# Kernel optimization log

Measured on AMD Instinct MI355X. Metric: run time of the kernel, lower is better.

## Reference

```python
import jax, jax.numpy as jnp
import numpy as np

N_NODES = 50000
N_EDGES = 600000
D_IN = 128
D_HID = 128


def _sage_conv(x, src, dst, W_l, b_l, W_r):
    """PyG SAGEConv (mean aggr): out = lin_l(mean_{j in N(i)} x_j) + lin_r(x_i).
    bias lives in lin_l only."""
    n = x.shape[0]
    agg = jax.ops.segment_sum(x[src], dst, num_segments=n)            # [N, D]
    cnt = jax.ops.segment_sum(jnp.ones((src.shape[0],), x.dtype), dst, num_segments=n)
    mean = agg / jnp.maximum(cnt, 1.0)[:, None]
    return mean @ W_l.T + b_l + x @ W_r.T


def setup_inputs() -> dict:
    key = jax.random.key(0)
    ks = jax.random.split(key, 8)
    glorot = lambda k, o, i: jax.random.normal(k, (o, i), jnp.float32) * np.sqrt(2.0 / (o + i))
    return {
        "x": jax.random.normal(ks[0], (N_NODES, D_IN), jnp.float32),
        "edge_index": jax.random.randint(ks[1], (2, N_EDGES), 0, N_NODES, jnp.int64),
        "W1_l": glorot(ks[2], D_HID, D_IN),
        "b1": jnp.zeros((D_HID,), jnp.float32),
        "W1_r": glorot(ks[3], D_HID, D_IN),
        "W2_l": glorot(ks[4], D_HID, D_HID),
        "b2": jnp.zeros((D_HID,), jnp.float32),
        "W2_r": glorot(ks[5], D_HID, D_HID),
    }


def reference(x, edge_index, W1_l, b1, W1_r, W2_l, b2, W2_r):
    src, dst = edge_index[0], edge_index[1]
    h = _sage_conv(x, src, dst, W1_l, b1, W1_r)
    h = jax.nn.leaky_relu(h, negative_slope=0.2)
    return _sage_conv(h, src, dst, W2_l, b2, W2_r)
```

## Files before the change

### kernel.cpp

```cpp
#include <hip/hip_runtime.h>

#define N_NODES 50000
#define N_EDGES 600000
#define D 128
#define CAP 64

typedef __attribute__((ext_vector_type(8))) short bf16x8;
typedef __attribute__((ext_vector_type(4))) float floatx4;

__device__ inline unsigned int f2bf(float f) {
    unsigned int u = __float_as_uint(f);
    return (u + 0x7FFFu + ((u >> 16) & 1u)) >> 16;
}
__device__ inline float bf_lo(unsigned int u) { return __uint_as_float(u << 16); }
__device__ inline float bf_hi(unsigned int u) { return __uint_as_float(u & 0xFFFF0000u); }

__global__ void k_prep(const float* __restrict__ x, unsigned short* __restrict__ xbf,
                       const float* __restrict__ wa, const float* __restrict__ wb,
                       const float* __restrict__ wc, const float* __restrict__ wd,
                       unsigned short* __restrict__ wbf,
                       const int* __restrict__ src, const int* __restrict__ dst,
                       int* __restrict__ cnt, unsigned short* __restrict__ buf,
                       int* __restrict__ spillN, int* __restrict__ spillD,
                       int* __restrict__ spillS) {
    const int b = blockIdx.x;
    const int t = threadIdx.x;
    if (b < 2344) {
        int e = b * 256 + t;
        if (e < N_EDGES) {
            int d = dst[e], s = src[e];
            int p = atomicAdd(&cnt[d], 1);
            if (p < CAP) {
                buf[(size_t)d * CAP + p] = (unsigned short)s;
            } else {
                int k = atomicAdd(spillN, 1);
                spillD[k] = d; spillS[k] = s;
            }
        }
    } else if (b < 8594) {
        int i = (b - 2344) * 256 + t;
        float4 v = ((const float4*)x)[i];
        uint2 o;
        o.x = f2bf(v.x) | (f2bf(v.y) << 16);
        o.y = f2bf(v.z) | (f2bf(v.w) << 16);
        ((uint2*)xbf)[i] = o;
    } else {
        int i = (b - 8594) * 256 + t;
        const float* srcs[4] = {wa, wb, wc, wd};
        wbf[i] = (unsigned short)f2bf(srcs[i >> 14][i & 16383]);
    }
}

#define ACC8(vv) do { \
    acc[0] += bf_lo((vv).x); acc[1] += bf_hi((vv).x); \
    acc[2] += bf_lo((vv).y); acc[3] += bf_hi((vv).y); \
    acc[4] += bf_lo((vv).z); acc[5] += bf_hi((vv).z); \
    acc[6] += bf_lo((vv).w); acc[7] += bf_hi((vv).w); } while (0)

template <bool RELU, bool OUT_BF16>
__global__ void __launch_bounds__(256) k_gather_layer(
    const int* __restrict__ cnt, const unsigned short* __restrict__ buf,
    const int* __restrict__ spillN, const int* __restrict__ spillD,
    const int* __restrict__ spillS,
    const unsigned short* __restrict__ Xbf,
    const unsigned short* __restrict__ Wlbf, const float* __restrict__ bias,
    const unsigned short* __restrict__ Wrbf, void* __restrict__ outp) {
    __shared__ unsigned short tile[16][136];

    const int t = threadIdx.x;
    const int node0 = blockIdx.x * 16;

    {
        const int nl = t >> 4, q = t & 15;
        const int node = node0 + nl;
        const int deg = cnt[node];
        const int m = deg < CAP ? deg : CAP;
        const unsigned short* __restrict__ nb = buf + (size_t)node * CAP;
        float acc[8] = {0.f, 0.f, 0.f, 0.f, 0.f, 0.f, 0.f, 0.f};
        int e = 0;
        for (; e + 8 <= m; e += 8) {
            uint4 v[8];
#pragma unroll
            for (int u = 0; u < 8; ++u)
                v[u] = *(const uint4*)(Xbf + (size_t)nb[e + u] * D + q * 8);
#pragma unroll
            for (int u = 0; u < 8; ++u) ACC8(v[u]);
        }
        for (; e + 4 <= m; e += 4) {
            uint4 v[4];
#pragma unroll
            for (int u = 0; u < 4; ++u)
                v[u] = *(const uint4*)(Xbf + (size_t)nb[e + u] * D + q * 8);
#pragma unroll
            for (int u = 0; u < 4; ++u) ACC8(v[u]);
        }
        for (; e < m; ++e) {
            uint4 v = *(const uint4*)(Xbf + (size_t)nb[e] * D + q * 8);
            ACC8(v);
        }
        if (deg > CAP) {
            int sn = *spillN;
            for (int k = 0; k < sn; ++k) {
                if (spillD[k] == node) {
                    uint4 v = *(const uint4*)(Xbf + (size_t)spillS[k] * D + q * 8);
                    ACC8(v);
                }
            }
        }
        float inv = (deg > 0) ? 1.0f / (float)deg : 0.0f;
        uint4 o;
        o.x = f2bf(acc[0] * inv) | (f2bf(acc[1] * inv) << 16);
        o.y = f2bf(acc[2] * inv) | (f2bf(acc[3] * inv) << 16);
        o.z = f2bf(acc[4] * inv) | (f2bf(acc[5] * inv) << 16);
        o.w = f2bf(acc[6] * inv) | (f2bf(acc[7] * inv) << 16);
        *(uint4*)(&tile[nl][q * 8]) = o;
    }
    __syncthreads();

    const int lane = t & 63;
    const int wv = t >> 6;
    const int l15 = lane & 15;
    const int quad = lane >> 4;

    floatx4 c0 = (floatx4)(0.f), c1 = (floatx4)(0.f);
    const int nf0 = wv * 2, nf1 = wv * 2 + 1;

    const unsigned short* mrow = &tile[l15][quad * 8];
    const unsigned short* arowX = Xbf + (size_t)(node0 + l15) * D + quad * 8;

#pragma unroll
    for (int kk = 0; kk < 4; ++kk) {
        bf16x8 a = *(const bf16x8*)(mrow + kk * 32);
        bf16x8 b0 = *(const bf16x8*)(Wlbf + (size_t)(nf0 * 16 + l15) * D + kk * 32 + quad * 8);
        bf16x8 b1 = *(const bf16x8*)(Wlbf + (size_t)(nf1 * 16 + l15) * D + kk * 32 + quad * 8);
        c0 = __builtin_amdgcn_mfma_f32_16x16x32_bf16(a, b0, c0, 0, 0, 0);
        c1 = __builtin_amdgcn_mfma_f32_16x16x32_bf16(a, b1, c1, 0, 0, 0);
    }
#pragma unroll
    for (int kk = 0; kk < 4; ++kk) {
        bf16x8 a = *(const bf16x8*)(arowX + kk * 32);
        bf16x8 b0 = *(const bf16x8*)(Wrbf + (size_t)(nf0 * 16 + l15) * D + kk * 32 + quad * 8);
        bf16x8 b1 = *(const bf16x8*)(Wrbf + (size_t)(nf1 * 16 + l15) * D + kk * 32 + quad * 8);
        c0 = __builtin_amdgcn_mfma_f32_16x16x32_bf16(a, b0, c0, 0, 0, 0);
        c1 = __builtin_amdgcn_mfma_f32_16x16x32_bf16(a, b1, c1, 0, 0, 0);
    }

#pragma unroll
    for (int j = 0; j < 2; ++j) {
        floatx4 c = j ? c1 : c0;
        int f = (wv * 2 + j) * 16 + l15;
        float bv = bias[f];
#pragma unroll
        for (int r = 0; r < 4; ++r) {
            float v = c[r] + bv;
            if (RELU) v = v > 0.f ? v : 0.2f * v;
            int node = node0 + quad * 4 + r;
            if (OUT_BF16)
                ((unsigned short*)outp)[(size_t)node * D + f] = (unsigned short)f2bf(v);
            else
                ((float*)outp)[(size_t)node * D + f] = v;
        }
    }
}


extern "C" void kernel_launch(void* const* d_in, const int* in_sizes, int n_in,
                              void* d_out, int out_size, void* d_ws, size_t ws_size,
                              hipStream_t stream) {
    (void)in_sizes; (void)n_in; (void)out_size; (void)ws_size;

    const float* x   = (const float*)d_in[0];
    const int*   ei  = (const int*)d_in[1];
    const float* W1l = (const float*)d_in[2];
    const float* b1  = (const float*)d_in[3];
    const float* W1r = (const float*)d_in[4];
    const float* W2l = (const float*)d_in[5];
    const float* b2  = (const float*)d_in[6];
    const float* W2r = (const float*)d_in[7];

    const int* src = ei;
    const int* dst = ei + N_EDGES;

    char* ws = (char*)d_ws;
    int* cnt              = (int*)(ws + 0);
    int* spillN           = (int*)(ws + 200000);
    int* spillD           = (int*)(ws + 200064);
    int* spillS           = (int*)(ws + 2600064);
    unsigned short* buf   = (unsigned short*)(ws + 5000064);
    unsigned short* wbf   = (unsigned short*)(ws + 11400064);
    unsigned short* hbf   = (unsigned short*)(ws + 11531136);

    unsigned short* xbf = (unsigned short*)d_out;
    float* out = (float*)d_out;

    unsigned short* w1l_bf = wbf;
    unsigned short* w1r_bf = wbf + 16384;
    unsigned short* w2l_bf = wbf + 32768;
    unsigned short* w2r_bf = wbf + 49152;

    hipMemsetAsync(ws, 0, 200064, stream);

    k_prep<<<8850, 256, 0, stream>>>(x, xbf, W1l, W1r, W2l, W2r, wbf,
                                     src, dst, cnt, buf, spillN, spillD, spillS);

    k_gather_layer<true, true><<<N_NODES / 16, 256, 0, stream>>>(
        cnt, buf, spillN, spillD, spillS, xbf, w1l_bf, b1, w1r_bf, (void*)hbf);
    k_gather_layer<false, false><<<N_NODES / 16, 256, 0, stream>>>(
        cnt, buf, spillN, spillD, spillS, hbf, w2l_bf, b2, w2r_bf, (void*)out);
}
```

Baseline: 223.7 us.

## Gather each node's neighbours with a full wavefront split four ways

The gather phase now gives each destination node a whole 64-lane wavefront, with 1024 threads per block, instead of 16 lanes. Each group of 16 lanes sums a quarter of the node's neighbour list, and the partial sums are combined with cross-lane shuffles. Neighbour ids are first staged in shared memory. The aim is more independent gather loads in flight per node, to hide random-access latency. In exchange, only a quarter of the threads take part in the MFMA projection, and the aggressive launch bounds may cap registers and cause spills.

Result: slower. 241.7 us (+8.1%).

```diff
diff --git a/kernel.cpp b/kernel.cpp
--- a/kernel.cpp
+++ b/kernel.cpp
@@ -58,7 +58,7 @@
     acc[6] += bf_lo((vv).w); acc[7] += bf_hi((vv).w); } while (0)
 
 template <bool RELU, bool OUT_BF16>
-__global__ void __launch_bounds__(256) k_gather_layer(
+__global__ void __launch_bounds__(1024, 8) k_gather_layer(
     const int* __restrict__ cnt, const unsigned short* __restrict__ buf,
     const int* __restrict__ spillN, const int* __restrict__ spillD,
     const int* __restrict__ spillS,
@@ -66,39 +66,46 @@
     const unsigned short* __restrict__ Wlbf, const float* __restrict__ bias,
     const unsigned short* __restrict__ Wrbf, void* __restrict__ outp) {
     __shared__ unsigned short tile[16][136];
+    __shared__ unsigned short lds_ids[16][64];
 
     const int t = threadIdx.x;
     const int node0 = blockIdx.x * 16;
 
     {
-        const int nl = t >> 4, q = t & 15;
-        const int node = node0 + nl;
+        const int wid = t >> 6;
+        const int lane = t & 63;
+        const int q = lane & 15;
+        const int par = lane >> 4;
+        const int node = node0 + wid;
         const int deg = cnt[node];
         const int m = deg < CAP ? deg : CAP;
-        const unsigned short* __restrict__ nb = buf + (size_t)node * CAP;
+
+        lds_ids[wid][lane] = buf[(size_t)node * CAP + lane];
+        const unsigned short* idr = &lds_ids[wid][0];
+
+        const int lo = (m * par) >> 2;
+        const int hi = (m * (par + 1)) >> 2;
+
         float acc[8] = {0.f, 0.f, 0.f, 0.f, 0.f, 0.f, 0.f, 0.f};
-        int e = 0;
-        for (; e + 8 <= m; e += 8) {
-            uint4 v[8];
-#pragma unroll
-            for (int u = 0; u < 8; ++u)
-                v[u] = *(const uint4*)(Xbf + (size_t)nb[e + u] * D + q * 8);
-#pragma unroll
-            for (int u = 0; u < 8; ++u) ACC8(v[u]);
-        }
-        for (; e + 4 <= m; e += 4) {
-            uint4 v[4];
-#pragma unroll
-            for (int u = 0; u < 4; ++u)
-                v[u] = *(const uint4*)(Xbf + (size_t)nb[e + u] * D + q * 8);
-#pragma unroll
-            for (int u = 0; u < 4; ++u) ACC8(v[u]);
-        }
-        for (; e < m; ++e) {
-            uint4 v = *(const uint4*)(Xbf + (size_t)nb[e] * D + q * 8);
-            ACC8(v);
-        }
-        if (deg > CAP) {
+        int e = lo;
+        for (; e + 4 <= hi; e += 4) {
+            uint4 v0 = *(const uint4*)(Xbf + (size_t)idr[e] * D + q * 8);
+            uint4 v1 = *(const uint4*)(Xbf + (size_t)idr[e + 1] * D + q * 8);
+            uint4 v2 = *(const uint4*)(Xbf + (size_t)idr[e + 2] * D + q * 8);
+            uint4 v3 = *(const uint4*)(Xbf + (size_t)idr[e + 3] * D + q * 8);
+            ACC8(v0); ACC8(v1); ACC8(v2); ACC8(v3);
+        }
+        {
+            int r = hi - e;
+            uint4 v0, v1, v2;
+            if (r > 0) v0 = *(const uint4*)(Xbf + (size_t)idr[e] * D + q * 8);
+            if (r > 1) v1 = *(const uint4*)(Xbf + (size_t)idr[e + 1] * D + q * 8);
+            if (r > 2) v2 = *(const uint4*)(Xbf + (size_t)idr[e + 2] * D + q * 8);
+            if (r > 0) ACC8(v0);
+            if (r > 1) ACC8(v1);
+            if (r > 2) ACC8(v2);
+        }
+        if (deg > CAP && par == 0) {
             int sn = *spillN;
             for (int k = 0; k < sn; ++k) {
                 if (spillD[k] == node) {
@@ -107,58 +114,67 @@
                 }
             }
         }
-        float inv = (deg > 0) ? 1.0f / (float)deg : 0.0f;
-        uint4 o;
-        o.x = f2bf(acc[0] * inv) | (f2bf(acc[1] * inv) << 16);
-        o.y = f2bf(acc[2] * inv) | (f2bf(acc[3] * inv) << 16);
-        o.z = f2bf(acc[4] * inv) | (f2bf(acc[5] * inv) << 16);
-        o.w = f2bf(acc[6] * inv) | (f2bf(acc[7] * inv) << 16);
-        *(uint4*)(&tile[nl][q * 8]) = o;
+#pragma unroll
+        for (int i = 0; i < 8; ++i) {
+            acc[i] += __shfl_xor(acc[i], 16, 64);
+            acc[i] += __shfl_xor(acc[i], 32, 64);
+        }
+        if (lane < 16) {
+            float inv = (deg > 0) ? 1.0f / (float)deg : 0.0f;
+            uint4 o;
+            o.x = f2bf(acc[0] * inv) | (f2bf(acc[1] * inv) << 16);
+            o.y = f2bf(acc[2] * inv) | (f2bf(acc[3] * inv) << 16);
+            o.z = f2bf(acc[4] * inv) | (f2bf(acc[5] * inv) << 16);
+            o.w = f2bf(acc[6] * inv) | (f2bf(acc[7] * inv) << 16);
+            *(uint4*)(&tile[wid][q * 8]) = o;
+        }
     }
     __syncthreads();
 
-    const int lane = t & 63;
-    const int wv = t >> 6;
-    const int l15 = lane & 15;
-    const int quad = lane >> 4;
-
-    floatx4 c0 = (floatx4)(0.f), c1 = (floatx4)(0.f);
-    const int nf0 = wv * 2, nf1 = wv * 2 + 1;
-
-    const unsigned short* mrow = &tile[l15][quad * 8];
-    const unsigned short* arowX = Xbf + (size_t)(node0 + l15) * D + quad * 8;
-
-#pragma unroll
-    for (int kk = 0; kk < 4; ++kk) {
-        bf16x8 a = *(const bf16x8*)(mrow + kk * 32);
-        bf16x8 b0 = *(const bf16x8*)(Wlbf + (size_t)(nf0 * 16 + l15) * D + kk * 32 + quad * 8);
-        bf16x8 b1 = *(const bf16x8*)(Wlbf + (size_t)(nf1 * 16 + l15) * D + kk * 32 + quad * 8);
-        c0 = __builtin_amdgcn_mfma_f32_16x16x32_bf16(a, b0, c0, 0, 0, 0);
-        c1 = __builtin_amdgcn_mfma_f32_16x16x32_bf16(a, b1, c1, 0, 0, 0);
-    }
-#pragma unroll
-    for (int kk = 0; kk < 4; ++kk) {
-        bf16x8 a = *(const bf16x8*)(arowX + kk * 32);
-        bf16x8 b0 = *(const bf16x8*)(Wrbf + (size_t)(nf0 * 16 + l15) * D + kk * 32 + quad * 8);
-        bf16x8 b1 = *(const bf16x8*)(Wrbf + (size_t)(nf1 * 16 + l15) * D + kk * 32 + quad * 8);
-        c0 = __builtin_amdgcn_mfma_f32_16x16x32_bf16(a, b0, c0, 0, 0, 0);
-        c1 = __builtin_amdgcn_mfma_f32_16x16x32_bf16(a, b1, c1, 0, 0, 0);
-    }
-
-#pragma unroll
-    for (int j = 0; j < 2; ++j) {
-        floatx4 c = j ? c1 : c0;
-        int f = (wv * 2 + j) * 16 + l15;
-        float bv = bias[f];
-#pragma unroll
-        for (int r = 0; r < 4; ++r) {
-            float v = c[r] + bv;
-            if (RELU) v = v > 0.f ? v : 0.2f * v;
-            int node = node0 + quad * 4 + r;
-            if (OUT_BF16)
-                ((unsigned short*)outp)[(size_t)node * D + f] = (unsigned short)f2bf(v);
-            else
-                ((float*)outp)[(size_t)node * D + f] = v;
+    if (t < 256) {
+        const int lane = t & 63;
+        const int wv = t >> 6;
+        const int l15 = lane & 15;
+        const int quad = lane >> 4;
+
+        floatx4 c0 = (floatx4)(0.f), c1 = (floatx4)(0.f);
+        const int nf0 = wv * 2, nf1 = wv * 2 + 1;
+
+        const unsigned short* mrow = &tile[l15][quad * 8];
+        const unsigned short* arowX = Xbf + (size_t)(node0 + l15) * D + quad * 8;
+
+#pragma unroll
+        for (int kk = 0; kk < 4; ++kk) {
+            bf16x8 a = *(const bf16x8*)(mrow + kk * 32);
+            bf16x8 b0 = *(const bf16x8*)(Wlbf + (size_t)(nf0 * 16 + l15) * D + kk * 32 + quad * 8);
+            bf16x8 b1 = *(const bf16x8*)(Wlbf + (size_t)(nf1 * 16 + l15) * D + kk * 32 + quad * 8);
+            c0 = __builtin_amdgcn_mfma_f32_16x16x32_bf16(a, b0, c0, 0, 0, 0);
+            c1 = __builtin_amdgcn_mfma_f32_16x16x32_bf16(a, b1, c1, 0, 0, 0);
+        }
+#pragma unroll
+        for (int kk = 0; kk < 4; ++kk) {
+            bf16x8 a = *(const bf16x8*)(arowX + kk * 32);
+            bf16x8 b0 = *(const bf16x8*)(Wrbf + (size_t)(nf0 * 16 + l15) * D + kk * 32 + quad * 8);
+            bf16x8 b1 = *(const bf16x8*)(Wrbf + (size_t)(nf1 * 16 + l15) * D + kk * 32 + quad * 8);
+            c0 = __builtin_amdgcn_mfma_f32_16x16x32_bf16(a, b0, c0, 0, 0, 0);
+            c1 = __builtin_amdgcn_mfma_f32_16x16x32_bf16(a, b1, c1, 0, 0, 0);
+        }
+
+#pragma unroll
+        for (int j = 0; j < 2; ++j) {
+            floatx4 c = j ? c1 : c0;
+            int f = (wv * 2 + j) * 16 + l15;
+            float bv = bias[f];
+#pragma unroll
+            for (int r = 0; r < 4; ++r) {
+                float v = c[r] + bv;
+                if (RELU) v = v > 0.f ? v : 0.2f * v;
+                int node = node0 + quad * 4 + r;
+                if (OUT_BF16)
+                    ((unsigned short*)outp)[(size_t)node * D + f] = (unsigned short)f2bf(v);
+                else
+                    ((float*)outp)[(size_t)node * D + f] = v;
+            }
         }
     }
 }
@@ -203,8 +219,8 @@
     k_prep<<<8850, 256, 0, stream>>>(x, xbf, W1l, W1r, W2l, W2r, wbf,
                                      src, dst, cnt, buf, spillN, spillD, spillS);
 
-    k_gather_layer<true, true><<<N_NODES / 16, 256, 0, stream>>>(
+    k_gather_layer<true, true><<<N_NODES / 16, 1024, 0, stream>>>(
         cnt, buf, spillN, spillD, spillS, xbf, w1l_bf, b1, w1r_bf, (void*)hbf);
-    k_gather_layer<false, false><<<N_NODES / 16, 256, 0, stream>>>(
+    k_gather_layer<false, false><<<N_NODES / 16, 1024, 0, stream>>>(
         cnt, buf, spillN, spillD, spillS, hbf, w2l_bf, b2, w2r_bf, (void*)out);
 }
```

## Fuse prep and both SAGE layers into one persistent cooperative kernel

Applied to the files above, without the earlier changes.

Replaces the memset plus three kernel launches with a single cooperative persistent kernel that zeroes the counters, builds the adjacency buckets, converts inputs to bf16, and runs both layers. The phases are separated by grid-wide syncs, and tiles are processed in grid-stride loops. This removes launch gaps and the separate memset, at the cost of grid barrier overhead and a grid capped by occupancy (at most 2048 blocks). A fallback to the old multi-kernel path remains if the cooperative launch fails.

Result: slower. 509.9 us (+128.0%).

```diff
diff --git a/kernel.cpp b/kernel.cpp
--- a/kernel.cpp
+++ b/kernel.cpp
@@ -1,9 +1,14 @@
 #include <hip/hip_runtime.h>
+#include <hip/hip_cooperative_groups.h>
+
+namespace cg = cooperative_groups;
 
 #define N_NODES 50000
 #define N_EDGES 600000
 #define D 128
 #define CAP 64
+#define NTILES (N_NODES / 16)
+#define SCAN_BLOCKS ((N_NODES + 255) / 256)
 
 typedef __attribute__((ext_vector_type(8))) short bf16x8;
 typedef __attribute__((ext_vector_type(4))) float floatx4;
@@ -14,6 +19,179 @@
 }
 __device__ inline float bf_lo(unsigned int u) { return __uint_as_float(u << 16); }
 __device__ inline float bf_hi(unsigned int u) { return __uint_as_float(u & 0xFFFF0000u); }
+
+#define ACC8(vv) do { \
+    acc[0] += bf_lo((vv).x); acc[1] += bf_hi((vv).x); \
+    acc[2] += bf_lo((vv).y); acc[3] += bf_hi((vv).y); \
+    acc[4] += bf_lo((vv).z); acc[5] += bf_hi((vv).z); \
+    acc[6] += bf_lo((vv).w); acc[7] += bf_hi((vv).w); } while (0)
+
+template <bool RELU, bool OUT_BF16>
+__device__ void layer_tile(int tileId, unsigned short (*tile)[136],
+                           const int* __restrict__ cnt, const unsigned short* __restrict__ buf,
+                           const int* __restrict__ spillN, const int* __restrict__ spillD,
+                           const int* __restrict__ spillS,
+                           const unsigned short* __restrict__ Xbf,
+                           const unsigned short* __restrict__ Wlbf, const float* __restrict__ bias,
+                           const unsigned short* __restrict__ Wrbf, void* __restrict__ outp) {
+    const int t = threadIdx.x;
+    const int node0 = tileId * 16;
+
+    {
+        const int nl = t >> 4, q = t & 15;
+        const int node = node0 + nl;
+        const int deg = cnt[node];
+        const int m = deg < CAP ? deg : CAP;
+        const unsigned short* __restrict__ nb = buf + (size_t)node * CAP;
+        float acc[8] = {0.f, 0.f, 0.f, 0.f, 0.f, 0.f, 0.f, 0.f};
+        int e = 0;
+        for (; e + 8 <= m; e += 8) {
+            uint4 v[8];
+#pragma unroll
+            for (int u = 0; u < 8; ++u)
+                v[u] = *(const uint4*)(Xbf + (size_t)nb[e + u] * D + q * 8);
+#pragma unroll
+            for (int u = 0; u < 8; ++u) ACC8(v[u]);
+        }
+        for (; e + 4 <= m; e += 4) {
+            uint4 v[4];
+#pragma unroll
+            for (int u = 0; u < 4; ++u)
+                v[u] = *(const uint4*)(Xbf + (size_t)nb[e + u] * D + q * 8);
+#pragma unroll
+            for (int u = 0; u < 4; ++u) ACC8(v[u]);
+        }
+        for (; e < m; ++e) {
+            uint4 v = *(const uint4*)(Xbf + (size_t)nb[e] * D + q * 8);
+            ACC8(v);
+        }
+        if (deg > CAP) {
+            int sn = *spillN;
+            for (int k = 0; k < sn; ++k) {
+                if (spillD[k] == node) {
+                    uint4 v = *(const uint4*)(Xbf + (size_t)spillS[k] * D + q * 8);
+                    ACC8(v);
+                }
+            }
+        }
+        float inv = (deg > 0) ? 1.0f / (float)deg : 0.0f;
+        uint4 o;
+        o.x = f2bf(acc[0] * inv) | (f2bf(acc[1] * inv) << 16);
+        o.y = f2bf(acc[2] * inv) | (f2bf(acc[3] * inv) << 16);
+        o.z = f2bf(acc[4] * inv) | (f2bf(acc[5] * inv) << 16);
+        o.w = f2bf(acc[6] * inv) | (f2bf(acc[7] * inv) << 16);
+        *(uint4*)(&tile[nl][q * 8]) = o;
+    }
+    __syncthreads();
+
+    {
+        const int lane = t & 63;
+        const int wv = t >> 6;
+        const int l15 = lane & 15;
+        const int quad = lane >> 4;
+
+        floatx4 c0 = (floatx4)(0.f), c1 = (floatx4)(0.f);
+        const int nf0 = wv * 2, nf1 = wv * 2 + 1;
+
+        const unsigned short* mrow = &tile[l15][quad * 8];
+        const unsigned short* arowX = Xbf + (size_t)(node0 + l15) * D + quad * 8;
+
+#pragma unroll
+        for (int kk = 0; kk < 4; ++kk) {
+            bf16x8 a = *(const bf16x8*)(mrow + kk * 32);
+            bf16x8 b0 = *(const bf16x8*)(Wlbf + (size_t)(nf0 * 16 + l15) * D + kk * 32 + quad * 8);
+            bf16x8 b1 = *(const bf16x8*)(Wlbf + (size_t)(nf1 * 16 + l15) * D + kk * 32 + quad * 8);
+            c0 = __builtin_amdgcn_mfma_f32_16x16x32_bf16(a, b0, c0, 0, 0, 0);
+            c1 = __builtin_amdgcn_mfma_f32_16x16x32_bf16(a, b1, c1, 0, 0, 0);
+        }
+#pragma unroll
+        for (int kk = 0; kk < 4; ++kk) {
+            bf16x8 a = *(const bf16x8*)(arowX + kk * 32);
+            bf16x8 b0 = *(const bf16x8*)(Wrbf + (size_t)(nf0 * 16 + l15) * D + kk * 32 + quad * 8);
+            bf16x8 b1 = *(const bf16x8*)(Wrbf + (size_t)(nf1 * 16 + l15) * D + kk * 32 + quad * 8);
+            c0 = __builtin_amdgcn_mfma_f32_16x16x32_bf16(a, b0, c0, 0, 0, 0);
+            c1 = __builtin_amdgcn_mfma_f32_16x16x32_bf16(a, b1, c1, 0, 0, 0);
+        }
+
+#pragma unroll
+        for (int j = 0; j < 2; ++j) {
+            floatx4 c = j ? c1 : c0;
+            int f = (wv * 2 + j) * 16 + l15;
+            float bv = bias[f];
+#pragma unroll
+            for (int r = 0; r < 4; ++r) {
+                float v = c[r] + bv;
+                if (RELU) v = v > 0.f ? v : 0.2f * v;
+                int node = node0 + quad * 4 + r;
+                if (OUT_BF16)
+                    ((unsigned short*)outp)[(size_t)node * D + f] = (unsigned short)f2bf(v);
+                else
+                    ((float*)outp)[(size_t)node * D + f] = v;
+            }
+        }
+    }
+    __syncthreads();
+}
+
+__global__ void __launch_bounds__(256, 8) k_fused(
+    const float* __restrict__ x, const int* __restrict__ src, const int* __restrict__ dst,
+    const float* __restrict__ W1l, const float* __restrict__ b1, const float* __restrict__ W1r,
+    const float* __restrict__ W2l, const float* __restrict__ b2, const float* __restrict__ W2r,
+    int* __restrict__ cnt, unsigned short* __restrict__ buf,
+    int* __restrict__ spillN, int* __restrict__ spillD, int* __restrict__ spillS,
+    unsigned short* __restrict__ wbf, unsigned short* xbf,
+    unsigned short* __restrict__ hbf, float* out) {
+    __shared__ unsigned short tile[16][136];
+
+    cg::grid_group grid = cg::this_grid();
+    const int t = threadIdx.x;
+    const int gid = blockIdx.x * 256 + t;
+    const int gsz = gridDim.x * 256;
+
+    for (int i = gid; i < N_NODES; i += gsz) cnt[i] = 0;
+    if (gid == 0) *spillN = 0;
+    __threadfence();
+    grid.sync();
+    __threadfence();
+
+    for (int e = gid; e < N_EDGES; e += gsz) {
+        int d = dst[e], s = src[e];
+        int p = atomicAdd(&cnt[d], 1);
+        if (p < CAP) {
+            buf[(size_t)d * CAP + p] = (unsigned short)s;
+        } else {
+            int k = atomicAdd(spillN, 1);
+            spillD[k] = d; spillS[k] = s;
+        }
+    }
+    for (int i = gid; i < N_NODES * D / 4; i += gsz) {
+        float4 v = ((const float4*)x)[i];
+        uint2 o;
+        o.x = f2bf(v.x) | (f2bf(v.y) << 16);
+        o.y = f2bf(v.z) | (f2bf(v.w) << 16);
+        ((uint2*)xbf)[i] = o;
+    }
+    for (int i = gid; i < 4 * D * D; i += gsz) {
+        int wsel = i >> 14, idx = i & 16383;
+        const float* p = wsel == 0 ? W1l : wsel == 1 ? W1r : wsel == 2 ? W2l : W2r;
+        wbf[i] = (unsigned short)f2bf(p[idx]);
+    }
+    __threadfence();
+    grid.sync();
+    __threadfence();
+
+    for (int tl = blockIdx.x; tl < NTILES; tl += gridDim.x)
+        layer_tile<true, true>(tl, tile, cnt, buf, spillN, spillD, spillS,
+                               xbf, wbf, b1, wbf + 16384, (void*)hbf);
+    __threadfence();
+    grid.sync();
+    __threadfence();
+
+    for (int tl = blockIdx.x; tl < NTILES; tl += gridDim.x)
+        layer_tile<false, false>(tl, tile, cnt, buf, spillN, spillD, spillS,
+                                 hbf, wbf + 32768, b2, wbf + 49152, (void*)out);
+}
+
 
 __global__ void k_prep(const float* __restrict__ x, unsigned short* __restrict__ xbf,
                        const float* __restrict__ wa, const float* __restrict__ wb,
@@ -51,12 +229,6 @@
     }
 }
 
-#define ACC8(vv) do { \
-    acc[0] += bf_lo((vv).x); acc[1] += bf_hi((vv).x); \
-    acc[2] += bf_lo((vv).y); acc[3] += bf_hi((vv).y); \
-    acc[4] += bf_lo((vv).z); acc[5] += bf_hi((vv).z); \
-    acc[6] += bf_lo((vv).w); acc[7] += bf_hi((vv).w); } while (0)
-
 template <bool RELU, bool OUT_BF16>
 __global__ void __launch_bounds__(256) k_gather_layer(
     const int* __restrict__ cnt, const unsigned short* __restrict__ buf,
@@ -66,101 +238,8 @@
     const unsigned short* __restrict__ Wlbf, const float* __restrict__ bias,
     const unsigned short* __restrict__ Wrbf, void* __restrict__ outp) {
     __shared__ unsigned short tile[16][136];
-
-    const int t = threadIdx.x;
-    const int node0 = blockIdx.x * 16;
-
-    {
-        const int nl = t >> 4, q = t & 15;
-        const int node = node0 + nl;
-        const int deg = cnt[node];
-        const int m = deg < CAP ? deg : CAP;
-        const unsigned short* __restrict__ nb = buf + (size_t)node * CAP;
-        float acc[8] = {0.f, 0.f, 0.f, 0.f, 0.f, 0.f, 0.f, 0.f};
-        int e = 0;
-        for (; e + 8 <= m; e += 8) {
-            uint4 v[8];
-#pragma unroll
-            for (int u = 0; u < 8; ++u)
-                v[u] = *(const uint4*)(Xbf + (size_t)nb[e + u] * D + q * 8);
-#pragma unroll
-            for (int u = 0; u < 8; ++u) ACC8(v[u]);
-        }
-        for (; e + 4 <= m; e += 4) {
-            uint4 v[4];
-#pragma unroll
-            for (int u = 0; u < 4; ++u)
-                v[u] = *(const uint4*)(Xbf + (size_t)nb[e + u] * D + q * 8);
-#pragma unroll
-            for (int u = 0; u < 4; ++u) ACC8(v[u]);
-        }
-        for (; e < m; ++e) {
-            uint4 v = *(const uint4*)(Xbf + (size_t)nb[e] * D + q * 8);
-            ACC8(v);
-        }
-        if (deg > CAP) {
-            int sn = *spillN;
-            for (int k = 0; k < sn; ++k) {
-                if (spillD[k] == node) {
-                    uint4 v = *(const uint4*)(Xbf + (size_t)spillS[k] * D + q * 8);
-                    ACC8(v);
-                }
-            }
-        }
-        float inv = (deg > 0) ? 1.0f / (float)deg : 0.0f;
-        uint4 o;
-        o.x = f2bf(acc[0] * inv) | (f2bf(acc[1] * inv) << 16);
-        o.y = f2bf(acc[2] * inv) | (f2bf(acc[3] * inv) << 16);
-        o.z = f2bf(acc[4] * inv) | (f2bf(acc[5] * inv) << 16);
-        o.w = f2bf(acc[6] * inv) | (f2bf(acc[7] * inv) << 16);
-        *(uint4*)(&tile[nl][q * 8]) = o;
-    }
-    __syncthreads();
-
-    const int lane = t & 63;
-    const int wv = t >> 6;
-    const int l15 = lane & 15;
-    const int quad = lane >> 4;
-
-    floatx4 c0 = (floatx4)(0.f), c1 = (floatx4)(0.f);
-    const int nf0 = wv * 2, nf1 = wv * 2 + 1;
-
-    const unsigned short* mrow = &tile[l15][quad * 8];
-    const unsigned short* arowX = Xbf + (size_t)(node0 + l15) * D + quad * 8;
-
-#pragma unroll
-    for (int kk = 0; kk < 4; ++kk) {
-        bf16x8 a = *(const bf16x8*)(mrow + kk * 32);
-        bf16x8 b0 = *(const bf16x8*)(Wlbf + (size_t)(nf0 * 16 + l15) * D + kk * 32 + quad * 8);
-        bf16x8 b1 = *(const bf16x8*)(Wlbf + (size_t)(nf1 * 16 + l15) * D + kk * 32 + quad * 8);
-        c0 = __builtin_amdgcn_mfma_f32_16x16x32_bf16(a, b0, c0, 0, 0, 0);
-        c1 = __builtin_amdgcn_mfma_f32_16x16x32_bf16(a, b1, c1, 0, 0, 0);
-    }
-#pragma unroll
-    for (int kk = 0; kk < 4; ++kk) {
-        bf16x8 a = *(const bf16x8*)(arowX + kk * 32);
-        bf16x8 b0 = *(const bf16x8*)(Wrbf + (size_t)(nf0 * 16 + l15) * D + kk * 32 + quad * 8);
-        bf16x8 b1 = *(const bf16x8*)(Wrbf + (size_t)(nf1 * 16 + l15) * D + kk * 32 + quad * 8);
-        c0 = __builtin_amdgcn_mfma_f32_16x16x32_bf16(a, b0, c0, 0, 0, 0);
-        c1 = __builtin_amdgcn_mfma_f32_16x16x32_bf16(a, b1, c1, 0, 0, 0);
-    }
-
-#pragma unroll
-    for (int j = 0; j < 2; ++j) {
-        floatx4 c = j ? c1 : c0;
-        int f = (wv * 2 + j) * 16 + l15;
-        float bv = bias[f];
-#pragma unroll
-        for (int r = 0; r < 4; ++r) {
-            float v = c[r] + bv;
-            if (RELU) v = v > 0.f ? v : 0.2f * v;
-            int node = node0 + quad * 4 + r;
-            if (OUT_BF16)
-                ((unsigned short*)outp)[(size_t)node * D + f] = (unsigned short)f2bf(v);
-            else
-                ((float*)outp)[(size_t)node * D + f] = v;
-        }
-    }
+    layer_tile<RELU, OUT_BF16>(blockIdx.x, tile, cnt, buf, spillN, spillD, spillS,
+                               Xbf, Wlbf, bias, Wrbf, outp);
 }
 
 
@@ -193,18 +272,49 @@
     unsigned short* xbf = (unsigned short*)d_out;
     float* out = (float*)d_out;
 
-    unsigned short* w1l_bf = wbf;
-    unsigned short* w1r_bf = wbf + 16384;
-    unsigned short* w2l_bf = wbf + 32768;
-    unsigned short* w2r_bf = wbf + 49152;
-
-    hipMemsetAsync(ws, 0, 200064, stream);
-
-    k_prep<<<8850, 256, 0, stream>>>(x, xbf, W1l, W1r, W2l, W2r, wbf,
-                                     src, dst, cnt, buf, spillN, spillD, spillS);
-
-    k_gather_layer<true, true><<<N_NODES / 16, 256, 0, stream>>>(
-        cnt, buf, spillN, spillD, spillS, xbf, w1l_bf, b1, w1r_bf, (void*)hbf);
-    k_gather_layer<false, false><<<N_NODES / 16, 256, 0, stream>>>(
-        cnt, buf, spillN, spillD, spillS, hbf, w2l_bf, b2, w2r_bf, (void*)out);
-}
+    static int coopBlocks = -2;
+    if (coopBlocks == -2) {
+        int perCU = 0, nCU = 0, dev = 0;
+        if (hipGetDevice(&dev) == hipSuccess &&
+            hipOccupancyMaxActiveBlocksPerMultiprocessor(&perCU, (const void*)k_fused,
+                                                         256, 0) == hipSuccess &&
+            hipDeviceGetAttribute(&nCU, hipDeviceAttributeMultiprocessorCount,
+                                  dev) == hipSuccess &&
+            perCU > 0 && nCU > 0) {
+            long long cap = (long long)perCU * (long long)nCU;
+            coopBlocks = (int)(cap < 2048 ? cap : 2048);
+        } else {
+            coopBlocks = -1;
+        }
+    }
+
+    bool done = false;
+    if (coopBlocks > 0) {
+        void* args[] = {
+            (void*)&x, (void*)&src, (void*)&dst,
+            (void*)&W1l, (void*)&b1, (void*)&W1r,
+            (void*)&W2l, (void*)&b2, (void*)&W2r,
+            (void*)&cnt, (void*)&buf,
+            (void*)&spillN, (void*)&spillD, (void*)&spillS,
+            (void*)&wbf, (void*)&xbf, (void*)&hbf, (void*)&out,
+        };
+        hipError_t err = hipLaunchCooperativeKernel((const void*)k_fused,
+                                                    dim3(coopBlocks), dim3(256),
+                                                    args, 0, stream);
+        if (err == hipSuccess) {
+            done = true;
+        } else {
+            (void)hipGetLastError();
+        }
+    }
+
+    if (!done) {
+        hipMemsetAsync(ws, 0, 200064, stream);
+        k_prep<<<8850, 256, 0, stream>>>(x, xbf, W1l, W1r, W2l, W2r, wbf,
+                                         src, dst, cnt, buf, spillN, spillD, spillS);
+        k_gather_layer<true, true><<<NTILES, 256, 0, stream>>>(
+            cnt, buf, spillN, spillD, spillS, xbf, wbf, b1, wbf + 16384, (void*)hbf);
+        k_gather_layer<false, false><<<NTILES, 256, 0, stream>>>(
+            cnt, buf, spillN, spillD, spillS, hbf, wbf + 32768, b2, wbf + 49152, (void*)out);
+    }
+}
```
